# Optimization experiments

Measured on AMD Instinct MI355X. Metric: run time of the kernel, lower is better.

## Reference

```python
import jax, jax.numpy as jnp
import numpy as np

N, D_MODEL, D_PE, H = 4096, 512, 16, 8


def setup_inputs() -> dict:
    key = jax.random.key(0)
    ks = jax.random.split(key, 6)
    s = 1.0 / np.sqrt(D_MODEL)
    return {
        "x": jax.random.normal(ks[0], (N, D_MODEL), dtype=jnp.float32),
        "pe": jax.random.normal(ks[1], (N, D_PE), dtype=jnp.float32),
        "w_qkv": jax.random.normal(ks[2], (D_MODEL, 3 * D_MODEL), dtype=jnp.float32) * s,
        "b_qkv": jnp.zeros((3 * D_MODEL,), dtype=jnp.float32),
        "w_pe": jax.random.normal(ks[3], (D_PE, H), dtype=jnp.float32) * (1.0 / np.sqrt(D_PE)),
        "b_pe": jnp.zeros((H,), dtype=jnp.float32),
        "w_out": jax.random.normal(ks[4], (D_MODEL, D_MODEL), dtype=jnp.float32) * s,
        "b_out": jnp.zeros((D_MODEL,), dtype=jnp.float32),
    }


def reference(x, pe, w_qkv, b_qkv, w_pe, b_pe, w_out, b_out):
    n, d = x.shape
    h = w_pe.shape[1]
    hd = d // h
    scale = hd ** -0.5

    qkv = (x @ w_qkv + b_qkv).reshape(n, 3, h, hd)  # [N,3,H,hd]
    q = jnp.transpose(qkv[:, 0], (1, 0, 2))  # [H,N,hd]
    k = jnp.transpose(qkv[:, 1], (1, 0, 2))
    v = jnp.transpose(qkv[:, 2], (1, 0, 2))

    pe_proj = pe @ w_pe + b_pe  # [N,H]
    # bias[h,i,j] = pe_proj[j,h] - pe_proj[i,h]  (matches torch unsqueeze/permute)
    pt = pe_proj.T  # [H,N]
    bias = pt[:, None, :] - pt[:, :, None]  # [H,N,N]

    scores = jnp.einsum('hnd,hmd->hnm', q, k) * scale + bias  # [H,N,N]
    attn = jax.nn.softmax(scores, axis=-1)
    out = jnp.einsum('hnm,hmd->hnd', attn, v)  # [H,N,hd]
    out = jnp.transpose(out, (1, 0, 2)).reshape(n, d)
    return out @ w_out + b_out
```

## Files before the change

kernel.cpp:

```cpp
#include <hip/hip_runtime.h>
#include <stdint.h>
#include <stddef.h>


typedef unsigned short u16;
typedef __attribute__((ext_vector_type(8))) short short8;
typedef __attribute__((ext_vector_type(8))) unsigned short us8;
typedef __attribute__((ext_vector_type(4))) unsigned short us4;
typedef __attribute__((ext_vector_type(4))) float floatx4;

__device__ __forceinline__ u16 f2b(float f) {
  union { float f; uint32_t u; } v; v.f = f;
  uint32_t u = v.u;
  return (u16)((u + 0x7fffu + ((u >> 16) & 1u)) >> 16);
}

__device__ __forceinline__ uint32_t pkbf16(float a, float b) {
  union { float f; uint32_t u; } x, y; x.f = a; y.f = b;
  return __builtin_amdgcn_perm(y.u + 0x8000u, x.u + 0x8000u, 0x07060302u);
}

#if __has_builtin(__builtin_amdgcn_exp2f)
__device__ __forceinline__ float fexp2(float x) { return __builtin_amdgcn_exp2f(x); }
#else
__device__ __forceinline__ float fexp2(float x) { return exp2f(x); }
#endif

__device__ __forceinline__ void gld16(const u16* g, u16* l) {
  __builtin_amdgcn_global_load_lds(
      (const __attribute__((address_space(1))) uint32_t*)(const void*)g,
      (__attribute__((address_space(3))) uint32_t*)(void*)l, 16, 0, 0);
}


__device__ __forceinline__ void tr_tile(const float* __restrict__ in,
                                        u16* __restrict__ out, int R, int C,
                                        int bx, int by, u16 (*tile)[33]) {
  int tx = threadIdx.x & 31, ty = threadIdx.x >> 5;
  int c0 = bx * 32, r0 = by * 32;
#pragma unroll
  for (int i = 0; i < 32; i += 8)
    tile[ty + i][tx] = f2b(in[(size_t)(r0 + ty + i) * C + c0 + tx]);
  __syncthreads();
#pragma unroll
  for (int i = 0; i < 32; i += 8)
    out[(size_t)(c0 + ty + i) * R + r0 + tx] = tile[tx][ty + i];
}

__global__ __launch_bounds__(256) void k_prep(
    const float* __restrict__ x, u16* __restrict__ xb,
    const float* __restrict__ w_qkv, u16* __restrict__ wqkvT,
    const float* __restrict__ w_out, u16* __restrict__ woutT,
    const float* __restrict__ pe, const float* __restrict__ w_pe,
    const float* __restrict__ b_pe, float* __restrict__ peT) {
  __shared__ u16 tile[32][33];
  int b = blockIdx.x;
  if (b < 2048) {
    int i = b * 256 + threadIdx.x;
    float4 v = ((const float4*)x)[i];
    uint2 o = make_uint2(pkbf16(v.x, v.y), pkbf16(v.z, v.w));
    ((uint2*)xb)[i] = o;
  } else if (b < 2816) {
    int idx = b - 2048;
    tr_tile(w_qkv, wqkvT, 512, 1536, idx % 48, idx / 48, tile);
  } else if (b < 3072) {
    int idx = b - 2816;
    tr_tile(w_out, woutT, 512, 512, idx % 16, idx / 16, tile);
  } else {
    int idx = (b - 3072) * 256 + threadIdx.x;
    int h = idx >> 12, n = idx & 4095;
    float acc = b_pe[h];
#pragma unroll
    for (int d = 0; d < 16; ++d) acc = fmaf(pe[n * 16 + d], w_pe[d * 8 + h], acc);
    peT[h * 4096 + n] = acc * 1.4426950408889634f - 16.0f;
  }
}


__global__ __launch_bounds__(512, 6) void k_gemm_qkv(const u16* __restrict__ A,
                                                     const u16* __restrict__ Bt,
                                                     const float* __restrict__ bias,
                                                     u16* __restrict__ qk,
                                                     u16* __restrict__ vtp) {
  __shared__ __align__(16) u16 smem[24576];
  const int tid = threadIdx.x;
  const int lane = tid & 63, wave = tid >> 6;
  const int colx = lane & 15, quad = lane >> 4;
  const int m0 = blockIdx.y * 64, n0 = blockIdx.x * 128;
  const int wm = wave >> 2, wn = wave & 3;
  const int sc = (lane & 7) ^ ((lane >> 3) & 7);
  const floatx4 fz = {0.f, 0.f, 0.f, 0.f};
  floatx4 acc[2][2];
#pragma unroll
  for (int i = 0; i < 2; ++i)
#pragma unroll
    for (int j = 0; j < 2; ++j) acc[i][j] = fz;

#define PREF_QKV(k0, b)                                                       \
  {                                                                           \
    int rowa = wave * 8 + (lane >> 3);                                        \
    gld16(&A[(size_t)(m0 + rowa) * 512 + (k0) + sc * 8],                      \
          &smem[(b) * 4096 + wave * 512 + lane * 8]);                         \
    _Pragma("unroll") for (int c = 0; c < 2; ++c) {                           \
      int rowb = wave * 16 + c * 8 + (lane >> 3);                             \
      gld16(&Bt[(size_t)(n0 + rowb) * 512 + (k0) + sc * 8],                   \
            &smem[8192 + (b) * 8192 + wave * 1024 + c * 512 + lane * 8]);     \
    }                                                                         \
  }

  PREF_QKV(0, 0);
  __syncthreads();
  for (int it = 0; it < 8; ++it) {
    int cur = it & 1;
    if (it < 7) PREF_QKV((it + 1) * 64, cur ^ 1);
    const u16* As = &smem[cur * 4096];
    const u16* Bs = &smem[8192 + cur * 8192];
#pragma unroll
    for (int kk = 0; kk < 2; ++kk) {
      short8 af[2], bf[2];
#pragma unroll
      for (int i = 0; i < 2; ++i) {
        int row = wm * 32 + i * 16 + colx;
        af[i] = *(const short8*)&As[row * 64 + (((kk * 4 + quad) ^ (colx & 7))) * 8];
      }
#pragma unroll
      for (int j = 0; j < 2; ++j) {
        int row = wn * 32 + j * 16 + colx;
        bf[j] = *(const short8*)&Bs[row * 64 + (((kk * 4 + quad) ^ (colx & 7))) * 8];
      }
#pragma unroll
      for (int i = 0; i < 2; ++i)
#pragma unroll
        for (int j = 0; j < 2; ++j)
          acc[i][j] = __builtin_amdgcn_mfma_f32_16x16x32_bf16(af[i], bf[j], acc[i][j], 0, 0, 0);
    }
    __syncthreads();
  }

  const bool isV = (blockIdx.x >= 8);
#pragma unroll
  for (int j = 0; j < 2; ++j) {
    int c = n0 + wn * 32 + j * 16 + colx;
    float bq = bias[c];
    if (!isV) {
#pragma unroll
      for (int i = 0; i < 2; ++i)
#pragma unroll
        for (int r = 0; r < 4; ++r) {
          int row = m0 + wm * 32 + i * 16 + quad * 4 + r;
          qk[(size_t)row * 1024 + c] = f2b(acc[i][j][r] + bq);
        }
    } else {
      int d = c - 1024;
#pragma unroll
      for (int i = 0; i < 2; ++i) {
        us4 o;
#pragma unroll
        for (int r = 0; r < 4; ++r) o[r] = f2b(acc[i][j][r] + bq);
        *(us4*)&vtp[(size_t)d * 4096 + m0 + wm * 32 + quad * 8 + i * 4] = o;
      }
    }
  }
#undef PREF_QKV
}


__global__ __launch_bounds__(512, 4) void k_gemm_out(const u16* __restrict__ A,
                                                     const u16* __restrict__ Bt,
                                                     const float* __restrict__ bias,
                                                     float* __restrict__ Cout) {
  __shared__ __align__(16) u16 smem[16384];
  const int tid = threadIdx.x;
  const int lane = tid & 63, wave = tid >> 6;
  const int colx = lane & 15, quad = lane >> 4;
  const int m0 = blockIdx.y * 64, n0 = blockIdx.x * 64;
  const int wm = wave >> 2, wn = wave & 3;
  const int sc = (lane & 7) ^ ((lane >> 3) & 7);
  const floatx4 fz = {0.f, 0.f, 0.f, 0.f};
  floatx4 acc[2];
  acc[0] = fz; acc[1] = fz;

#define PREF_OUT(k0, b)                                                       \
  {                                                                           \
    int rowa = wave * 8 + (lane >> 3);                                        \
    gld16(&A[(size_t)(m0 + rowa) * 512 + (k0) + sc * 8],                      \
          &smem[(b) * 4096 + wave * 512 + lane * 8]);                         \
    gld16(&Bt[(size_t)(n0 + rowa) * 512 + (k0) + sc * 8],                     \
          &smem[8192 + (b) * 4096 + wave * 512 + lane * 8]);                  \
  }

  PREF_OUT(0, 0);
  __syncthreads();
  for (int it = 0; it < 8; ++it) {
    int cur = it & 1;
    if (it < 7) PREF_OUT((it + 1) * 64, cur ^ 1);
    const u16* As = &smem[cur * 4096];
    const u16* Bs = &smem[8192 + cur * 4096];
#pragma unroll
    for (int kk = 0; kk < 2; ++kk) {
      short8 af[2], bf;
#pragma unroll
      for (int i = 0; i < 2; ++i) {
        int row = wm * 32 + i * 16 + colx;
        af[i] = *(const short8*)&As[row * 64 + (((kk * 4 + quad) ^ (colx & 7))) * 8];
      }
      {
        int row = wn * 16 + colx;
        bf = *(const short8*)&Bs[row * 64 + (((kk * 4 + quad) ^ (colx & 7))) * 8];
      }
#pragma unroll
      for (int i = 0; i < 2; ++i)
        acc[i] = __builtin_amdgcn_mfma_f32_16x16x32_bf16(af[i], bf, acc[i], 0, 0, 0);
    }
    __syncthreads();
  }
  int c = n0 + wn * 16 + colx;
  float bq = bias[c];
#pragma unroll
  for (int i = 0; i < 2; ++i)
#pragma unroll
    for (int r = 0; r < 4; ++r) {
      int row = m0 + wm * 32 + i * 16 + quad * 4 + r;
      Cout[(size_t)row * 512 + c] = acc[i][r] + bq;
    }
#undef PREF_OUT
}


__global__ __launch_bounds__(512, 8) void k_flash(const u16* __restrict__ qk,
                                                  const u16* __restrict__ vt,
                                                  const float* __restrict__ peT,
                                                  float* __restrict__ opart,
                                                  float* __restrict__ lpart) {
  __shared__ __align__(16) u16 smem[20480];
  float* bufs = (float*)smem;

  const int tid = threadIdx.x;
  const int lane = tid & 63, wave = tid >> 6;
  const int colx = lane & 15, quad = lane >> 4;
  const int ih = wave >> 1, jq = wave & 1;
  const int q0 = blockIdx.x * 64;
  const int h = blockIdx.y;
  const int z = blockIdx.z;
  const int kvb = z * 2048;
  const float sscale = 0.125f * 1.4426950408889634f;
  const floatx4 fz = {0.f, 0.f, 0.f, 0.f};

  const int sc = (lane & 7) ^ ((lane >> 3) & 7);
  const int srow = wave * 8 + (lane >> 3);

#define PREF_F(j0n, b)                                                        \
  {                                                                           \
    gld16(&qk[(size_t)(kvb + (j0n) + srow) * 1024 + 512 + h * 64 + sc * 8],   \
          &smem[4096 + (b) * 4096 + wave * 512 + lane * 8]);                  \
    gld16(&vt[(size_t)(h * 64 + srow) * 4096 + kvb + (j0n) + sc * 8],         \
          &smem[12288 + (b) * 4096 + wave * 512 + lane * 8]);                 \
  }

  {
    int row = tid >> 3, ch = tid & 7;
    *(us8*)&smem[row * 64 + (ch ^ (row & 7)) * 8] =
        *(const us8*)&qk[(size_t)(q0 + row) * 1024 + h * 64 + ch * 8];
  }
  PREF_F(0, 0);
  __syncthreads();

  short8 qf[2];
#pragma unroll
  for (int kk = 0; kk < 2; ++kk) {
    int row = ih * 16 + colx;
    qf[kk] = *(const short8*)&smem[row * 64 + (((kk * 4 + quad) ^ (colx & 7))) * 8];
  }

  floatx4 oacc[4];
#pragma unroll
  for (int cb = 0; cb < 4; ++cb) oacc[cb] = fz;
  float rsum = 0.0f;

  for (int it = 0; it < 32; ++it) {
    const int cur = it & 1;
    if (it < 31) PREF_F((it + 1) * 64, cur ^ 1);
    const u16* Ks = &smem[4096 + cur * 4096];
    const u16* Vts = &smem[12288 + cur * 4096];

    floatx4 pev[2];
#pragma unroll
    for (int j2 = 0; j2 < 2; ++j2)
      pev[j2] = *(const floatx4*)&peT[h * 4096 + kvb + it * 64 + jq * 32 + j2 * 16 + quad * 4];

    floatx4 sacc[2] = {fz, fz};
#pragma unroll
    for (int j2 = 0; j2 < 2; ++j2) {
#pragma unroll
      for (int kk = 0; kk < 2; ++kk) {
        int row = jq * 32 + j2 * 16 + colx;
        short8 kf = *(const short8*)&Ks[row * 64 + (((kk * 4 + quad) ^ (colx & 7))) * 8];
        sacc[j2] = __builtin_amdgcn_mfma_f32_16x16x32_bf16(kf, qf[kk], sacc[j2], 0, 0, 0);
      }
    }
    union { uint32_t w[4]; short8 s; } pk;
#pragma unroll
    for (int j2 = 0; j2 < 2; ++j2) {
      float p0 = fexp2(fmaf(sacc[j2][0], sscale, pev[j2][0]));
      float p1 = fexp2(fmaf(sacc[j2][1], sscale, pev[j2][1]));
      float p2 = fexp2(fmaf(sacc[j2][2], sscale, pev[j2][2]));
      float p3 = fexp2(fmaf(sacc[j2][3], sscale, pev[j2][3]));
      rsum += (p0 + p1) + (p2 + p3);
      pk.w[j2 * 2 + 0] = pkbf16(p0, p1);
      pk.w[j2 * 2 + 1] = pkbf16(p2, p3);
    }
#pragma unroll
    for (int cb = 0; cb < 4; ++cb) {
      int row = cb * 16 + colx;
      short8 vf = *(const short8*)&Vts[row * 64 + (((jq * 4 + quad) ^ (colx & 7))) * 8];
      oacc[cb] = __builtin_amdgcn_mfma_f32_16x16x32_bf16(pk.s, vf, oacc[cb], 0, 0, 0);
    }
    __syncthreads();
  }

  rsum += __shfl_xor(rsum, 16);
  rsum += __shfl_xor(rsum, 32);

  float* b = bufs + ih * 1040;
  if (jq == 1) {
#pragma unroll
    for (int cb = 0; cb < 4; ++cb)
#pragma unroll
      for (int r = 0; r < 4; ++r)
        b[(quad * 4 + r) * 65 + cb * 16 + colx] = oacc[cb][r];
    if (quad == 0) b[colx * 65 + 64] = rsum;
  }
  __syncthreads();
  if (jq == 0) {
#pragma unroll
    for (int cb = 0; cb < 4; ++cb)
#pragma unroll
      for (int r = 0; r < 4; ++r)
        oacc[cb][r] += b[(quad * 4 + r) * 65 + cb * 16 + colx];
    rsum += b[colx * 65 + 64];
    float* op = opart + (size_t)z * 2097152;
#pragma unroll
    for (int cb = 0; cb < 4; ++cb)
#pragma unroll
      for (int r = 0; r < 4; ++r)
        op[(size_t)(q0 + ih * 16 + quad * 4 + r) * 512 + h * 64 + cb * 16 + colx] =
            oacc[cb][r];
    if (quad == 0)
      lpart[z * 32768 + h * 4096 + q0 + ih * 16 + colx] = rsum;
  }
#undef PREF_F
}


__global__ __launch_bounds__(256) void k_comb(const float* __restrict__ opart,
                                              const float* __restrict__ lpart,
                                              u16* __restrict__ ao) {
  int idx = blockIdx.x * 256 + threadIdx.x;
  int n = idx >> 7, d4 = idx & 127;
  int h = d4 >> 4;
  float l = lpart[h * 4096 + n] + lpart[32768 + h * 4096 + n];
  float inv = 1.0f / l;
  float4 o0 = *(const float4*)&opart[(size_t)n * 512 + d4 * 4];
  float4 o1 = *(const float4*)&opart[2097152 + (size_t)n * 512 + d4 * 4];
  us4 o;
  o[0] = f2b((o0.x + o1.x) * inv);
  o[1] = f2b((o0.y + o1.y) * inv);
  o[2] = f2b((o0.z + o1.z) * inv);
  o[3] = f2b((o0.w + o1.w) * inv);
  *(us4*)&ao[(size_t)n * 512 + d4 * 4] = o;
}


extern "C" void kernel_launch(void* const* d_in, const int* in_sizes, int n_in,
                              void* d_out, int out_size, void* d_ws, size_t ws_size,
                              hipStream_t stream) {
  const float* x     = (const float*)d_in[0];
  const float* pe    = (const float*)d_in[1];
  const float* w_qkv = (const float*)d_in[2];
  const float* b_qkv = (const float*)d_in[3];
  const float* w_pe  = (const float*)d_in[4];
  const float* b_pe  = (const float*)d_in[5];
  const float* w_out = (const float*)d_in[6];
  const float* b_out = (const float*)d_in[7];
  float* out = (float*)d_out;

  u16* xb    = (u16*)d_ws;
  u16* wqkvT = xb    + 2097152;
  u16* woutT = wqkvT + 786432;
  u16* qk    = woutT + 262144;
  u16* vt    = qk    + 4194304;
  u16* ao    = vt    + 2097152;
  float* peT   = (float*)(ao + 2097152);
  float* opart = peT + 32768;
  float* lpart = opart + 4194304;

  k_prep<<<3200, 256, 0, stream>>>(x, xb, w_qkv, wqkvT, w_out, woutT,
                                   pe, w_pe, b_pe, peT);
  k_gemm_qkv<<<dim3(12, 64), 512, 0, stream>>>(xb, wqkvT, b_qkv, qk, vt);
  k_flash<<<dim3(64, 8, 2), 512, 0, stream>>>(qk, vt, peT, opart, lpart);
  k_comb<<<2048, 256, 0, stream>>>(opart, lpart, ao);
  k_gemm_out<<<dim3(8, 64), 512, 0, stream>>>(ao, woutT, b_out, out);
}
```

Baseline: 152.5 us.

## Fold positional bias into V weights, MFMA row sums, fuse combine into out GEMM

Because bias[i,j] = p[j] - p[i], the per-query term cancels in softmax and the per-key term becomes a multiplicative weight exp(p[j]). The change folds that weight into V in the QKV GEMM epilogue and folds the score scale into Q. The flash loop therefore drops its per-tile peT loads and FMAs, and the softmax denominator is computed with an extra MFMA against a bf16 weight vector instead of scalar adds. The separate combine kernel is removed by normalising and merging the split-K partials while loading A tiles in the output GEMM. The cost is extra bf16 rounding of the weights and of the scaled V and Q, and A tiles in the out GEMM are now loaded synchronously through registers.

Result: slower. 159.8 us (+4.8%).

```diff
diff --git a/kernel.cpp b/kernel.cpp
--- a/kernel.cpp
+++ b/kernel.cpp
@@ -52,7 +52,8 @@
     const float* __restrict__ w_qkv, u16* __restrict__ wqkvT,
     const float* __restrict__ w_out, u16* __restrict__ woutT,
     const float* __restrict__ pe, const float* __restrict__ w_pe,
-    const float* __restrict__ b_pe, float* __restrict__ peT) {
+    const float* __restrict__ b_pe, float* __restrict__ wexp,
+    u16* __restrict__ wpb) {
   __shared__ u16 tile[32][33];
   int b = blockIdx.x;
   if (b < 2048) {
@@ -72,7 +73,12 @@
     float acc = b_pe[h];
 #pragma unroll
     for (int d = 0; d < 16; ++d) acc = fmaf(pe[n * 16 + d], w_pe[d * 8 + h], acc);
-    peT[h * 4096 + n] = acc * 1.4426950408889634f - 16.0f;
+    float w = exp2f(acc * 1.4426950408889634f - 16.0f);
+    u16 wb = f2b(w);
+    union { uint32_t u; float f; } cv; cv.u = ((uint32_t)wb) << 16;
+    wexp[h * 4096 + n] = cv.f;
+    int pn = (n & ~31) | (((n >> 2) & 3) << 3) | (((n >> 4) & 1) << 2) | (n & 3);
+    wpb[h * 4096 + pn] = wb;
   }
 }
 
@@ -80,6 +86,7 @@
 __global__ __launch_bounds__(512, 6) void k_gemm_qkv(const u16* __restrict__ A,
                                                      const u16* __restrict__ Bt,
                                                      const float* __restrict__ bias,
+                                                     const float* __restrict__ wexp,
                                                      u16* __restrict__ qk,
                                                      u16* __restrict__ vtp) {
   __shared__ __align__(16) u16 smem[24576];
@@ -143,20 +150,25 @@
     int c = n0 + wn * 32 + j * 16 + colx;
     float bq = bias[c];
     if (!isV) {
+      float qs = (c < 512) ? 0.18033688011112042f : 1.0f;
 #pragma unroll
       for (int i = 0; i < 2; ++i)
 #pragma unroll
         for (int r = 0; r < 4; ++r) {
           int row = m0 + wm * 32 + i * 16 + quad * 4 + r;
-          qk[(size_t)row * 1024 + c] = f2b(acc[i][j][r] + bq);
+          qk[(size_t)row * 1024 + c] = f2b((acc[i][j][r] + bq) * qs);
         }
     } else {
       int d = c - 1024;
+      int hh = (n0 + wn * 32 + j * 16 - 1024) >> 6;
 #pragma unroll
       for (int i = 0; i < 2; ++i) {
         us4 o;
 #pragma unroll
-        for (int r = 0; r < 4; ++r) o[r] = f2b(acc[i][j][r] + bq);
+        for (int r = 0; r < 4; ++r) {
+          int na = m0 + wm * 32 + i * 16 + quad * 4 + r;
+          o[r] = f2b((acc[i][j][r] + bq) * wexp[hh * 4096 + na]);
+        }
         *(us4*)&vtp[(size_t)d * 4096 + m0 + wm * 32 + quad * 8 + i * 4] = o;
       }
     }
@@ -165,7 +177,136 @@
 }
 
 
-__global__ __launch_bounds__(512, 4) void k_gemm_out(const u16* __restrict__ A,
+__global__ __launch_bounds__(512, 8) void k_flash(const u16* __restrict__ qk,
+                                                  const u16* __restrict__ vt,
+                                                  const u16* __restrict__ wpb,
+                                                  float* __restrict__ opart,
+                                                  float* __restrict__ lpart) {
+  __shared__ __align__(16) u16 smem[20480];
+  float* bufs = (float*)smem;
+
+  const int tid = threadIdx.x;
+  const int lane = tid & 63, wave = tid >> 6;
+  const int colx = lane & 15, quad = lane >> 4;
+  const int ih = wave >> 1, jq = wave & 1;
+  const int q0 = blockIdx.x * 64;
+  const int h = blockIdx.y;
+  const int z = blockIdx.z;
+  const int kvb = z * 2048;
+  const floatx4 fz = {0.f, 0.f, 0.f, 0.f};
+
+  const int sc = (lane & 7) ^ ((lane >> 3) & 7);
+  const int srow = wave * 8 + (lane >> 3);
+
+#define PREF_F(j0n, b)                                                        \
+  {                                                                           \
+    gld16(&qk[(size_t)(kvb + (j0n) + srow) * 1024 + 512 + h * 64 + sc * 8],   \
+          &smem[4096 + (b) * 4096 + wave * 512 + lane * 8]);                  \
+    gld16(&vt[(size_t)(h * 64 + srow) * 4096 + kvb + (j0n) + sc * 8],         \
+          &smem[12288 + (b) * 4096 + wave * 512 + lane * 8]);                 \
+  }
+
+  {
+    int row = tid >> 3, ch = tid & 7;
+    *(us8*)&smem[row * 64 + (ch ^ (row & 7)) * 8] =
+        *(const us8*)&qk[(size_t)(q0 + row) * 1024 + h * 64 + ch * 8];
+  }
+  PREF_F(0, 0);
+  __syncthreads();
+
+  short8 qf[2];
+#pragma unroll
+  for (int kk = 0; kk < 2; ++kk) {
+    int row = ih * 16 + colx;
+    qf[kk] = *(const short8*)&smem[row * 64 + (((kk * 4 + quad) ^ (colx & 7))) * 8];
+  }
+
+  const u16* wbase = wpb + h * 4096 + kvb + jq * 32 + quad * 8;
+  short8 wf = *(const short8*)wbase;
+
+  floatx4 oacc[4], lacc = fz;
+#pragma unroll
+  for (int cb = 0; cb < 4; ++cb) oacc[cb] = fz;
+
+  for (int it = 0; it < 32; ++it) {
+    const int cur = it & 1;
+    short8 wfn;
+    if (it < 31) {
+      PREF_F((it + 1) * 64, cur ^ 1);
+      wfn = *(const short8*)&wbase[(it + 1) * 64];
+    }
+    const u16* Ks = &smem[4096 + cur * 4096];
+    const u16* Vts = &smem[12288 + cur * 4096];
+
+    floatx4 sacc[2] = {fz, fz};
+#pragma unroll
+    for (int j2 = 0; j2 < 2; ++j2) {
+#pragma unroll
+      for (int kk = 0; kk < 2; ++kk) {
+        int row = jq * 32 + j2 * 16 + colx;
+        short8 kf = *(const short8*)&Ks[row * 64 + (((kk * 4 + quad) ^ (colx & 7))) * 8];
+        sacc[j2] = __builtin_amdgcn_mfma_f32_16x16x32_bf16(kf, qf[kk], sacc[j2], 0, 0, 0);
+      }
+    }
+    union { uint32_t w[4]; short8 s; } pk;
+#pragma unroll
+    for (int j2 = 0; j2 < 2; ++j2) {
+      float p0 = fexp2(sacc[j2][0]);
+      float p1 = fexp2(sacc[j2][1]);
+      float p2 = fexp2(sacc[j2][2]);
+      float p3 = fexp2(sacc[j2][3]);
+      pk.w[j2 * 2 + 0] = pkbf16(p0, p1);
+      pk.w[j2 * 2 + 1] = pkbf16(p2, p3);
+    }
+#pragma unroll
+    for (int cb = 0; cb < 4; ++cb) {
+      int row = cb * 16 + colx;
+      short8 vf = *(const short8*)&Vts[row * 64 + (((jq * 4 + quad) ^ (colx & 7))) * 8];
+      oacc[cb] = __builtin_amdgcn_mfma_f32_16x16x32_bf16(pk.s, vf, oacc[cb], 0, 0, 0);
+    }
+    lacc = __builtin_amdgcn_mfma_f32_16x16x32_bf16(pk.s, wf, lacc, 0, 0, 0);
+    if (it < 31) wf = wfn;
+    __syncthreads();
+  }
+
+  float* b = bufs + ih * 1040;
+  if (jq == 1) {
+#pragma unroll
+    for (int cb = 0; cb < 4; ++cb)
+#pragma unroll
+      for (int r = 0; r < 4; ++r)
+        b[(quad * 4 + r) * 65 + cb * 16 + colx] = oacc[cb][r];
+    if (colx == 0)
+#pragma unroll
+      for (int r = 0; r < 4; ++r) b[(quad * 4 + r) * 65 + 64] = lacc[r];
+  }
+  __syncthreads();
+  if (jq == 0) {
+#pragma unroll
+    for (int cb = 0; cb < 4; ++cb)
+#pragma unroll
+      for (int r = 0; r < 4; ++r)
+        oacc[cb][r] += b[(quad * 4 + r) * 65 + cb * 16 + colx];
+#pragma unroll
+    for (int r = 0; r < 4; ++r) lacc[r] += b[(quad * 4 + r) * 65 + 64];
+    float* op = opart + (size_t)z * 2097152;
+#pragma unroll
+    for (int cb = 0; cb < 4; ++cb)
+#pragma unroll
+      for (int r = 0; r < 4; ++r)
+        op[(size_t)(q0 + ih * 16 + quad * 4 + r) * 512 + h * 64 + cb * 16 + colx] =
+            oacc[cb][r];
+    if (colx == 0)
+#pragma unroll
+      for (int r = 0; r < 4; ++r)
+        lpart[z * 32768 + h * 4096 + q0 + ih * 16 + quad * 4 + r] = lacc[r];
+  }
+#undef PREF_F
+}
+
+
+__global__ __launch_bounds__(512, 4) void k_gemm_out(const float* __restrict__ opart,
+                                                     const float* __restrict__ lpart,
                                                      const u16* __restrict__ Bt,
                                                      const float* __restrict__ bias,
                                                      float* __restrict__ Cout) {
@@ -176,24 +317,42 @@
   const int m0 = blockIdx.y * 64, n0 = blockIdx.x * 64;
   const int wm = wave >> 2, wn = wave & 3;
   const int sc = (lane & 7) ^ ((lane >> 3) & 7);
+  const int rowa = wave * 8 + (lane >> 3);
+  const int na = m0 + rowa;
   const floatx4 fz = {0.f, 0.f, 0.f, 0.f};
   floatx4 acc[2];
   acc[0] = fz; acc[1] = fz;
 
-#define PREF_OUT(k0, b)                                                       \
+#define LOADA(k0)                                                             \
   {                                                                           \
-    int rowa = wave * 8 + (lane >> 3);                                        \
-    gld16(&A[(size_t)(m0 + rowa) * 512 + (k0) + sc * 8],                      \
-          &smem[(b) * 4096 + wave * 512 + lane * 8]);                         \
-    gld16(&Bt[(size_t)(n0 + rowa) * 512 + (k0) + sc * 8],                     \
-          &smem[8192 + (b) * 4096 + wave * 512 + lane * 8]);                  \
-  }
-
-  PREF_OUT(0, 0);
+    int dbase = (k0) + sc * 8;                                                \
+    const float4* p0 = (const float4*)&opart[(size_t)na * 512 + dbase];       \
+    const float4* p1 = (const float4*)&opart[2097152 + (size_t)na * 512 + dbase]; \
+    a0 = p0[0]; a1 = p0[1]; c0 = p1[0]; c1 = p1[1];                           \
+    int hh = dbase >> 6;                                                      \
+    li = 1.0f / (lpart[hh * 4096 + na] + lpart[32768 + hh * 4096 + na]);      \
+  }
+#define PACKA(b)                                                              \
+  {                                                                           \
+    union { uint32_t w[4]; us8 v; } pa;                                       \
+    pa.w[0] = pkbf16((a0.x + c0.x) * li, (a0.y + c0.y) * li);                 \
+    pa.w[1] = pkbf16((a0.z + c0.z) * li, (a0.w + c0.w) * li);                 \
+    pa.w[2] = pkbf16((a1.x + c1.x) * li, (a1.y + c1.y) * li);                 \
+    pa.w[3] = pkbf16((a1.z + c1.z) * li, (a1.w + c1.w) * li);                 \
+    *(us8*)&smem[(b) * 4096 + wave * 512 + lane * 8] = pa.v;                  \
+  }
+
+  float4 a0, a1, c0, c1; float li;
+  LOADA(0); PACKA(0);
+  gld16(&Bt[(size_t)(n0 + rowa) * 512 + sc * 8], &smem[8192 + wave * 512 + lane * 8]);
   __syncthreads();
   for (int it = 0; it < 8; ++it) {
     int cur = it & 1;
-    if (it < 7) PREF_OUT((it + 1) * 64, cur ^ 1);
+    if (it < 7) {
+      LOADA((it + 1) * 64);
+      gld16(&Bt[(size_t)(n0 + rowa) * 512 + (it + 1) * 64 + sc * 8],
+            &smem[8192 + (cur ^ 1) * 4096 + wave * 512 + lane * 8]);
+    }
     const u16* As = &smem[cur * 4096];
     const u16* Bs = &smem[8192 + cur * 4096];
 #pragma unroll
@@ -212,6 +371,7 @@
       for (int i = 0; i < 2; ++i)
         acc[i] = __builtin_amdgcn_mfma_f32_16x16x32_bf16(af[i], bf, acc[i], 0, 0, 0);
     }
+    if (it < 7) PACKA(cur ^ 1);
     __syncthreads();
   }
   int c = n0 + wn * 16 + colx;
@@ -223,151 +383,8 @@
       int row = m0 + wm * 32 + i * 16 + quad * 4 + r;
       Cout[(size_t)row * 512 + c] = acc[i][r] + bq;
     }
-#undef PREF_OUT
-}
-
-
-__global__ __launch_bounds__(512, 8) void k_flash(const u16* __restrict__ qk,
-                                                  const u16* __restrict__ vt,
-                                                  const float* __restrict__ peT,
-                                                  float* __restrict__ opart,
-                                                  float* __restrict__ lpart) {
-  __shared__ __align__(16) u16 smem[20480];
-  float* bufs = (float*)smem;
-
-  const int tid = threadIdx.x;
-  const int lane = tid & 63, wave = tid >> 6;
-  const int colx = lane & 15, quad = lane >> 4;
-  const int ih = wave >> 1, jq = wave & 1;
-  const int q0 = blockIdx.x * 64;
-  const int h = blockIdx.y;
-  const int z = blockIdx.z;
-  const int kvb = z * 2048;
-  const float sscale = 0.125f * 1.4426950408889634f;
-  const floatx4 fz = {0.f, 0.f, 0.f, 0.f};
-
-  const int sc = (lane & 7) ^ ((lane >> 3) & 7);
-  const int srow = wave * 8 + (lane >> 3);
-
-#define PREF_F(j0n, b)                                                        \
-  {                                                                           \
-    gld16(&qk[(size_t)(kvb + (j0n) + srow) * 1024 + 512 + h * 64 + sc * 8],   \
-          &smem[4096 + (b) * 4096 + wave * 512 + lane * 8]);                  \
-    gld16(&vt[(size_t)(h * 64 + srow) * 4096 + kvb + (j0n) + sc * 8],         \
-          &smem[12288 + (b) * 4096 + wave * 512 + lane * 8]);                 \
-  }
-
-  {
-    int row = tid >> 3, ch = tid & 7;
-    *(us8*)&smem[row * 64 + (ch ^ (row & 7)) * 8] =
-        *(const us8*)&qk[(size_t)(q0 + row) * 1024 + h * 64 + ch * 8];
-  }
-  PREF_F(0, 0);
-  __syncthreads();
-
-  short8 qf[2];
-#pragma unroll
-  for (int kk = 0; kk < 2; ++kk) {
-    int row = ih * 16 + colx;
-    qf[kk] = *(const short8*)&smem[row * 64 + (((kk * 4 + quad) ^ (colx & 7))) * 8];
-  }
-
-  floatx4 oacc[4];
-#pragma unroll
-  for (int cb = 0; cb < 4; ++cb) oacc[cb] = fz;
-  float rsum = 0.0f;
-
-  for (int it = 0; it < 32; ++it) {
-    const int cur = it & 1;
-    if (it < 31) PREF_F((it + 1) * 64, cur ^ 1);
-    const u16* Ks = &smem[4096 + cur * 4096];
-    const u16* Vts = &smem[12288 + cur * 4096];
-
-    floatx4 pev[2];
-#pragma unroll
-    for (int j2 = 0; j2 < 2; ++j2)
-      pev[j2] = *(const floatx4*)&peT[h * 4096 + kvb + it * 64 + jq * 32 + j2 * 16 + quad * 4];
-
-    floatx4 sacc[2] = {fz, fz};
-#pragma unroll
-    for (int j2 = 0; j2 < 2; ++j2) {
-#pragma unroll
-      for (int kk = 0; kk < 2; ++kk) {
-        int row = jq * 32 + j2 * 16 + colx;
-        short8 kf = *(const short8*)&Ks[row * 64 + (((kk * 4 + quad) ^ (colx & 7))) * 8];
-        sacc[j2] = __builtin_amdgcn_mfma_f32_16x16x32_bf16(kf, qf[kk], sacc[j2], 0, 0, 0);
-      }
-    }
-    union { uint32_t w[4]; short8 s; } pk;
-#pragma unroll
-    for (int j2 = 0; j2 < 2; ++j2) {
-      float p0 = fexp2(fmaf(sacc[j2][0], sscale, pev[j2][0]));
-      float p1 = fexp2(fmaf(sacc[j2][1], sscale, pev[j2][1]));
-      float p2 = fexp2(fmaf(sacc[j2][2], sscale, pev[j2][2]));
-      float p3 = fexp2(fmaf(sacc[j2][3], sscale, pev[j2][3]));
-      rsum += (p0 + p1) + (p2 + p3);
-      pk.w[j2 * 2 + 0] = pkbf16(p0, p1);
-      pk.w[j2 * 2 + 1] = pkbf16(p2, p3);
-    }
-#pragma unroll
-    for (int cb = 0; cb < 4; ++cb) {
-      int row = cb * 16 + colx;
-      short8 vf = *(const short8*)&Vts[row * 64 + (((jq * 4 + quad) ^ (colx & 7))) * 8];
-      oacc[cb] = __builtin_amdgcn_mfma_f32_16x16x32_bf16(pk.s, vf, oacc[cb], 0, 0, 0);
-    }
-    __syncthreads();
-  }
-
-  rsum += __shfl_xor(rsum, 16);
-  rsum += __shfl_xor(rsum, 32);
-
-  float* b = bufs + ih * 1040;
-  if (jq == 1) {
-#pragma unroll
-    for (int cb = 0; cb < 4; ++cb)
-#pragma unroll
-      for (int r = 0; r < 4; ++r)
-        b[(quad * 4 + r) * 65 + cb * 16 + colx] = oacc[cb][r];
-    if (quad == 0) b[colx * 65 + 64] = rsum;
-  }
-  __syncthreads();
-  if (jq == 0) {
-#pragma unroll
-    for (int cb = 0; cb < 4; ++cb)
-#pragma unroll
-      for (int r = 0; r < 4; ++r)
-        oacc[cb][r] += b[(quad * 4 + r) * 65 + cb * 16 + colx];
-    rsum += b[colx * 65 + 64];
-    float* op = opart + (size_t)z * 2097152;
-#pragma unroll
-    for (int cb = 0; cb < 4; ++cb)
-#pragma unroll
-      for (int r = 0; r < 4; ++r)
-        op[(size_t)(q0 + ih * 16 + quad * 4 + r) * 512 + h * 64 + cb * 16 + colx] =
-            oacc[cb][r];
-    if (quad == 0)
-      lpart[z * 32768 + h * 4096 + q0 + ih * 16 + colx] = rsum;
-  }
-#undef PREF_F
-}
-
-
-__global__ __launch_bounds__(256) void k_comb(const float* __restrict__ opart,
-                                              const float* __restrict__ lpart,
-                                              u16* __restrict__ ao) {
-  int idx = blockIdx.x * 256 + threadIdx.x;
-  int n = idx >> 7, d4 = idx & 127;
-  int h = d4 >> 4;
-  float l = lpart[h * 4096 + n] + lpart[32768 + h * 4096 + n];
-  float inv = 1.0f / l;
-  float4 o0 = *(const float4*)&opart[(size_t)n * 512 + d4 * 4];
-  float4 o1 = *(const float4*)&opart[2097152 + (size_t)n * 512 + d4 * 4];
-  us4 o;
-  o[0] = f2b((o0.x + o1.x) * inv);
-  o[1] = f2b((o0.y + o1.y) * inv);
-  o[2] = f2b((o0.z + o1.z) * inv);
-  o[3] = f2b((o0.w + o1.w) * inv);
-  *(us4*)&ao[(size_t)n * 512 + d4 * 4] = o;
+#undef LOADA
+#undef PACKA
 }
 
 
@@ -389,15 +406,14 @@
   u16* woutT = wqkvT + 786432;
   u16* qk    = woutT + 262144;
   u16* vt    = qk    + 4194304;
-  u16* ao    = vt    + 2097152;
-  float* peT   = (float*)(ao + 2097152);
-  float* opart = peT + 32768;
+  u16* wpb   = vt    + 2097152;
+  float* wexp  = (float*)(wpb + 32768);
+  float* opart = wexp + 32768;
   float* lpart = opart + 4194304;
 
   k_prep<<<3200, 256, 0, stream>>>(x, xb, w_qkv, wqkvT, w_out, woutT,
-                                   pe, w_pe, b_pe, peT);
-  k_gemm_qkv<<<dim3(12, 64), 512, 0, stream>>>(xb, wqkvT, b_qkv, qk, vt);
-  k_flash<<<dim3(64, 8, 2), 512, 0, stream>>>(qk, vt, peT, opart, lpart);
-  k_comb<<<2048, 256, 0, stream>>>(opart, lpart, ao);
-  k_gemm_out<<<dim3(8, 64), 512, 0, stream>>>(ao, woutT, b_out, out);
-}
+                                   pe, w_pe, b_pe, wexp, wpb);
+  k_gemm_qkv<<<dim3(12, 64), 512, 0, stream>>>(xb, wqkvT, b_qkv, wexp, qk, vt);
+  k_flash<<<dim3(64, 8, 2), 512, 0, stream>>>(qk, vt, wpb, opart, lpart);
+  k_gemm_out<<<dim3(8, 64), 512, 0, stream>>>(opart, lpart, woutT, b_out, out);
+}
```

## Fold positional bias into V scaling and compute row sums via MFMA

Applied to the files above, without the earlier changes.

The positional bias pe_proj[j]-pe_proj[i] is factored out of the softmax. The key-side term becomes an exp weight folded into V during the QKV GEMM epilogue. The query-side term cancels under normalization. The softmax scale is folded into Q, so the flash inner loop drops the per-element FMA and bias loads. Row sums are computed by an extra MFMA against a permuted bf16 weight vector instead of scalar adds, and the main loop is unrolled by two with pointer increments. The cost is extra bf16 rounding of the weights and scaled V, plus one more MFMA per tile.

New measurement: 146.4 us. -4.0%, faster.

```diff
diff --git a/kernel.cpp b/kernel.cpp
--- a/kernel.cpp
+++ b/kernel.cpp
@@ -52,7 +52,8 @@
     const float* __restrict__ w_qkv, u16* __restrict__ wqkvT,
     const float* __restrict__ w_out, u16* __restrict__ woutT,
     const float* __restrict__ pe, const float* __restrict__ w_pe,
-    const float* __restrict__ b_pe, float* __restrict__ peT) {
+    const float* __restrict__ b_pe, float* __restrict__ wexp,
+    u16* __restrict__ wpb) {
   __shared__ u16 tile[32][33];
   int b = blockIdx.x;
   if (b < 2048) {
@@ -72,7 +73,12 @@
     float acc = b_pe[h];
 #pragma unroll
     for (int d = 0; d < 16; ++d) acc = fmaf(pe[n * 16 + d], w_pe[d * 8 + h], acc);
-    peT[h * 4096 + n] = acc * 1.4426950408889634f - 16.0f;
+    float w = exp2f(acc * 1.4426950408889634f - 16.0f);
+    u16 wb = f2b(w);
+    union { uint32_t u; float f; } cv; cv.u = ((uint32_t)wb) << 16;
+    wexp[h * 4096 + n] = cv.f;
+    int pn = (n & ~31) | (((n >> 2) & 3) << 3) | (((n >> 4) & 1) << 2) | (n & 3);
+    wpb[h * 4096 + pn] = wb;
   }
 }
 
@@ -80,6 +86,7 @@
 __global__ __launch_bounds__(512, 6) void k_gemm_qkv(const u16* __restrict__ A,
                                                      const u16* __restrict__ Bt,
                                                      const float* __restrict__ bias,
+                                                     const float* __restrict__ wexp,
                                                      u16* __restrict__ qk,
                                                      u16* __restrict__ vtp) {
   __shared__ __align__(16) u16 smem[24576];
@@ -138,17 +145,25 @@
   }
 
   const bool isV = (blockIdx.x >= 8);
+  floatx4 wv[2];
+  if (isV) {
+    int hh = (n0 + wn * 32 - 1024) >> 6;
+#pragma unroll
+    for (int i = 0; i < 2; ++i)
+      wv[i] = *(const floatx4*)&wexp[hh * 4096 + m0 + wm * 32 + i * 16 + quad * 4];
+  }
 #pragma unroll
   for (int j = 0; j < 2; ++j) {
     int c = n0 + wn * 32 + j * 16 + colx;
     float bq = bias[c];
     if (!isV) {
+      float qs = (c < 512) ? 0.18033688011112042f : 1.0f;
 #pragma unroll
       for (int i = 0; i < 2; ++i)
 #pragma unroll
         for (int r = 0; r < 4; ++r) {
           int row = m0 + wm * 32 + i * 16 + quad * 4 + r;
-          qk[(size_t)row * 1024 + c] = f2b(acc[i][j][r] + bq);
+          qk[(size_t)row * 1024 + c] = f2b((acc[i][j][r] + bq) * qs);
         }
     } else {
       int d = c - 1024;
@@ -156,7 +171,8 @@
       for (int i = 0; i < 2; ++i) {
         us4 o;
 #pragma unroll
-        for (int r = 0; r < 4; ++r) o[r] = f2b(acc[i][j][r] + bq);
+        for (int r = 0; r < 4; ++r)
+          o[r] = f2b((acc[i][j][r] + bq) * wv[i][r]);
         *(us4*)&vtp[(size_t)d * 4096 + m0 + wm * 32 + quad * 8 + i * 4] = o;
       }
     }
@@ -165,71 +181,9 @@
 }
 
 
-__global__ __launch_bounds__(512, 4) void k_gemm_out(const u16* __restrict__ A,
-                                                     const u16* __restrict__ Bt,
-                                                     const float* __restrict__ bias,
-                                                     float* __restrict__ Cout) {
-  __shared__ __align__(16) u16 smem[16384];
-  const int tid = threadIdx.x;
-  const int lane = tid & 63, wave = tid >> 6;
-  const int colx = lane & 15, quad = lane >> 4;
-  const int m0 = blockIdx.y * 64, n0 = blockIdx.x * 64;
-  const int wm = wave >> 2, wn = wave & 3;
-  const int sc = (lane & 7) ^ ((lane >> 3) & 7);
-  const floatx4 fz = {0.f, 0.f, 0.f, 0.f};
-  floatx4 acc[2];
-  acc[0] = fz; acc[1] = fz;
-
-#define PREF_OUT(k0, b)                                                       \
-  {                                                                           \
-    int rowa = wave * 8 + (lane >> 3);                                        \
-    gld16(&A[(size_t)(m0 + rowa) * 512 + (k0) + sc * 8],                      \
-          &smem[(b) * 4096 + wave * 512 + lane * 8]);                         \
-    gld16(&Bt[(size_t)(n0 + rowa) * 512 + (k0) + sc * 8],                     \
-          &smem[8192 + (b) * 4096 + wave * 512 + lane * 8]);                  \
-  }
-
-  PREF_OUT(0, 0);
-  __syncthreads();
-  for (int it = 0; it < 8; ++it) {
-    int cur = it & 1;
-    if (it < 7) PREF_OUT((it + 1) * 64, cur ^ 1);
-    const u16* As = &smem[cur * 4096];
-    const u16* Bs = &smem[8192 + cur * 4096];
-#pragma unroll
-    for (int kk = 0; kk < 2; ++kk) {
-      short8 af[2], bf;
-#pragma unroll
-      for (int i = 0; i < 2; ++i) {
-        int row = wm * 32 + i * 16 + colx;
-        af[i] = *(const short8*)&As[row * 64 + (((kk * 4 + quad) ^ (colx & 7))) * 8];
-      }
-      {
-        int row = wn * 16 + colx;
-        bf = *(const short8*)&Bs[row * 64 + (((kk * 4 + quad) ^ (colx & 7))) * 8];
-      }
-#pragma unroll
-      for (int i = 0; i < 2; ++i)
-        acc[i] = __builtin_amdgcn_mfma_f32_16x16x32_bf16(af[i], bf, acc[i], 0, 0, 0);
-    }
-    __syncthreads();
-  }
-  int c = n0 + wn * 16 + colx;
-  float bq = bias[c];
-#pragma unroll
-  for (int i = 0; i < 2; ++i)
-#pragma unroll
-    for (int r = 0; r < 4; ++r) {
-      int row = m0 + wm * 32 + i * 16 + quad * 4 + r;
-      Cout[(size_t)row * 512 + c] = acc[i][r] + bq;
-    }
-#undef PREF_OUT
-}
-
-
 __global__ __launch_bounds__(512, 8) void k_flash(const u16* __restrict__ qk,
                                                   const u16* __restrict__ vt,
-                                                  const float* __restrict__ peT,
+                                                  const u16* __restrict__ wpb,
                                                   float* __restrict__ opart,
                                                   float* __restrict__ lpart) {
   __shared__ __align__(16) u16 smem[20480];
@@ -243,26 +197,23 @@
   const int h = blockIdx.y;
   const int z = blockIdx.z;
   const int kvb = z * 2048;
-  const float sscale = 0.125f * 1.4426950408889634f;
   const floatx4 fz = {0.f, 0.f, 0.f, 0.f};
 
   const int sc = (lane & 7) ^ ((lane >> 3) & 7);
   const int srow = wave * 8 + (lane >> 3);
-
-#define PREF_F(j0n, b)                                                        \
-  {                                                                           \
-    gld16(&qk[(size_t)(kvb + (j0n) + srow) * 1024 + 512 + h * 64 + sc * 8],   \
-          &smem[4096 + (b) * 4096 + wave * 512 + lane * 8]);                  \
-    gld16(&vt[(size_t)(h * 64 + srow) * 4096 + kvb + (j0n) + sc * 8],         \
-          &smem[12288 + (b) * 4096 + wave * 512 + lane * 8]);                 \
-  }
 
   {
     int row = tid >> 3, ch = tid & 7;
     *(us8*)&smem[row * 64 + (ch ^ (row & 7)) * 8] =
         *(const us8*)&qk[(size_t)(q0 + row) * 1024 + h * 64 + ch * 8];
   }
-  PREF_F(0, 0);
+  const u16* qptr = qk + (size_t)(kvb + srow) * 1024 + 512 + h * 64 + sc * 8;
+  const u16* vptr = vt + (size_t)(h * 64 + srow) * 4096 + kvb + sc * 8;
+  const u16* wptr = wpb + h * 4096 + kvb + jq * 32 + quad * 8;
+  gld16(qptr, &smem[4096 + wave * 512 + lane * 8]);
+  gld16(vptr, &smem[12288 + wave * 512 + lane * 8]);
+  qptr += 65536;
+  vptr += 64;
   __syncthreads();
 
   short8 qf[2];
@@ -272,54 +223,59 @@
     qf[kk] = *(const short8*)&smem[row * 64 + (((kk * 4 + quad) ^ (colx & 7))) * 8];
   }
 
-  floatx4 oacc[4];
+  floatx4 oacc[4], lacc = fz;
 #pragma unroll
   for (int cb = 0; cb < 4; ++cb) oacc[cb] = fz;
-  float rsum = 0.0f;
-
-  for (int it = 0; it < 32; ++it) {
-    const int cur = it & 1;
-    if (it < 31) PREF_F((it + 1) * 64, cur ^ 1);
-    const u16* Ks = &smem[4096 + cur * 4096];
-    const u16* Vts = &smem[12288 + cur * 4096];
-
-    floatx4 pev[2];
-#pragma unroll
-    for (int j2 = 0; j2 < 2; ++j2)
-      pev[j2] = *(const floatx4*)&peT[h * 4096 + kvb + it * 64 + jq * 32 + j2 * 16 + quad * 4];
-
-    floatx4 sacc[2] = {fz, fz};
-#pragma unroll
-    for (int j2 = 0; j2 < 2; ++j2) {
-#pragma unroll
-      for (int kk = 0; kk < 2; ++kk) {
-        int row = jq * 32 + j2 * 16 + colx;
-        short8 kf = *(const short8*)&Ks[row * 64 + (((kk * 4 + quad) ^ (colx & 7))) * 8];
-        sacc[j2] = __builtin_amdgcn_mfma_f32_16x16x32_bf16(kf, qf[kk], sacc[j2], 0, 0, 0);
-      }
-    }
-    union { uint32_t w[4]; short8 s; } pk;
-#pragma unroll
-    for (int j2 = 0; j2 < 2; ++j2) {
-      float p0 = fexp2(fmaf(sacc[j2][0], sscale, pev[j2][0]));
-      float p1 = fexp2(fmaf(sacc[j2][1], sscale, pev[j2][1]));
-      float p2 = fexp2(fmaf(sacc[j2][2], sscale, pev[j2][2]));
-      float p3 = fexp2(fmaf(sacc[j2][3], sscale, pev[j2][3]));
-      rsum += (p0 + p1) + (p2 + p3);
-      pk.w[j2 * 2 + 0] = pkbf16(p0, p1);
-      pk.w[j2 * 2 + 1] = pkbf16(p2, p3);
-    }
-#pragma unroll
-    for (int cb = 0; cb < 4; ++cb) {
-      int row = cb * 16 + colx;
-      short8 vf = *(const short8*)&Vts[row * 64 + (((jq * 4 + quad) ^ (colx & 7))) * 8];
-      oacc[cb] = __builtin_amdgcn_mfma_f32_16x16x32_bf16(pk.s, vf, oacc[cb], 0, 0, 0);
-    }
-    __syncthreads();
-  }
-
-  rsum += __shfl_xor(rsum, 16);
-  rsum += __shfl_xor(rsum, 32);
+
+#define FBODY(CUR, PREF)                                                      \
+  {                                                                           \
+    short8 wf = *(const short8*)wptr;                                         \
+    wptr += 64;                                                               \
+    if (PREF) {                                                               \
+      gld16(qptr, &smem[4096 + (1 - (CUR)) * 4096 + wave * 512 + lane * 8]);  \
+      gld16(vptr, &smem[12288 + (1 - (CUR)) * 4096 + wave * 512 + lane * 8]); \
+      qptr += 65536;                                                          \
+      vptr += 64;                                                             \
+    }                                                                         \
+    const u16* Ks = &smem[4096 + (CUR) * 4096];                               \
+    const u16* Vts = &smem[12288 + (CUR) * 4096];                             \
+    floatx4 sacc[2] = {fz, fz};                                               \
+    _Pragma("unroll") for (int j2 = 0; j2 < 2; ++j2) {                        \
+      _Pragma("unroll") for (int kk = 0; kk < 2; ++kk) {                      \
+        int row = jq * 32 + j2 * 16 + colx;                                   \
+        short8 kf = *(const short8*)&Ks[row * 64 +                            \
+                                        (((kk * 4 + quad) ^ (colx & 7))) * 8];\
+        sacc[j2] =                                                            \
+            __builtin_amdgcn_mfma_f32_16x16x32_bf16(kf, qf[kk], sacc[j2], 0, 0, 0); \
+      }                                                                       \
+    }                                                                         \
+    union { uint32_t w[4]; short8 s; } pk;                                    \
+    _Pragma("unroll") for (int j2 = 0; j2 < 2; ++j2) {                        \
+      float p0 = fexp2(sacc[j2][0]);                                          \
+      float p1 = fexp2(sacc[j2][1]);                                          \
+      float p2 = fexp2(sacc[j2][2]);                                          \
+      float p3 = fexp2(sacc[j2][3]);                                          \
+      pk.w[j2 * 2 + 0] = pkbf16(p0, p1);                                      \
+      pk.w[j2 * 2 + 1] = pkbf16(p2, p3);                                      \
+    }                                                                         \
+    _Pragma("unroll") for (int cb = 0; cb < 4; ++cb) {                        \
+      int row = cb * 16 + colx;                                               \
+      short8 vf = *(const short8*)&Vts[row * 64 +                             \
+                                       (((jq * 4 + quad) ^ (colx & 7))) * 8]; \
+      oacc[cb] =                                                              \
+          __builtin_amdgcn_mfma_f32_16x16x32_bf16(pk.s, vf, oacc[cb], 0, 0, 0); \
+    }                                                                         \
+    lacc = __builtin_amdgcn_mfma_f32_16x16x32_bf16(pk.s, wf, lacc, 0, 0, 0);  \
+    __syncthreads();                                                          \
+  }
+
+  for (int t = 0; t < 15; ++t) {
+    FBODY(0, 1)
+    FBODY(1, 1)
+  }
+  FBODY(0, 1)
+  FBODY(1, 0)
+#undef FBODY
 
   float* b = bufs + ih * 1040;
   if (jq == 1) {
@@ -328,7 +284,9 @@
 #pragma unroll
       for (int r = 0; r < 4; ++r)
         b[(quad * 4 + r) * 65 + cb * 16 + colx] = oacc[cb][r];
-    if (quad == 0) b[colx * 65 + 64] = rsum;
+    if (colx == 0)
+#pragma unroll
+      for (int r = 0; r < 4; ++r) b[(quad * 4 + r) * 65 + 64] = lacc[r];
   }
   __syncthreads();
   if (jq == 0) {
@@ -337,7 +295,8 @@
 #pragma unroll
       for (int r = 0; r < 4; ++r)
         oacc[cb][r] += b[(quad * 4 + r) * 65 + cb * 16 + colx];
-    rsum += b[colx * 65 + 64];
+#pragma unroll
+    for (int r = 0; r < 4; ++r) lacc[r] += b[(quad * 4 + r) * 65 + 64];
     float* op = opart + (size_t)z * 2097152;
 #pragma unroll
     for (int cb = 0; cb < 4; ++cb)
@@ -345,10 +304,11 @@
       for (int r = 0; r < 4; ++r)
         op[(size_t)(q0 + ih * 16 + quad * 4 + r) * 512 + h * 64 + cb * 16 + colx] =
             oacc[cb][r];
-    if (quad == 0)
-      lpart[z * 32768 + h * 4096 + q0 + ih * 16 + colx] = rsum;
-  }
-#undef PREF_F
+    if (colx == 0)
+#pragma unroll
+      for (int r = 0; r < 4; ++r)
+        lpart[z * 32768 + h * 4096 + q0 + ih * 16 + quad * 4 + r] = lacc[r];
+  }
 }
 
 
@@ -371,6 +331,68 @@
 }
 
 
+__global__ __launch_bounds__(512, 4) void k_gemm_out(const u16* __restrict__ A,
+                                                     const u16* __restrict__ Bt,
+                                                     const float* __restrict__ bias,
+                                                     float* __restrict__ Cout) {
+  __shared__ __align__(16) u16 smem[16384];
+  const int tid = threadIdx.x;
+  const int lane = tid & 63, wave = tid >> 6;
+  const int colx = lane & 15, quad = lane >> 4;
+  const int m0 = blockIdx.y * 64, n0 = blockIdx.x * 64;
+  const int wm = wave >> 2, wn = wave & 3;
+  const int sc = (lane & 7) ^ ((lane >> 3) & 7);
+  const floatx4 fz = {0.f, 0.f, 0.f, 0.f};
+  floatx4 acc[2];
+  acc[0] = fz; acc[1] = fz;
+
+#define PREF_OUT(k0, b)                                                       \
+  {                                                                           \
+    int rowa = wave * 8 + (lane >> 3);                                        \
+    gld16(&A[(size_t)(m0 + rowa) * 512 + (k0) + sc * 8],                      \
+          &smem[(b) * 4096 + wave * 512 + lane * 8]);                         \
+    gld16(&Bt[(size_t)(n0 + rowa) * 512 + (k0) + sc * 8],                     \
+          &smem[8192 + (b) * 4096 + wave * 512 + lane * 8]);                  \
+  }
+
+  PREF_OUT(0, 0);
+  __syncthreads();
+  for (int it = 0; it < 8; ++it) {
+    int cur = it & 1;
+    if (it < 7) PREF_OUT((it + 1) * 64, cur ^ 1);
+    const u16* As = &smem[cur * 4096];
+    const u16* Bs = &smem[8192 + cur * 4096];
+#pragma unroll
+    for (int kk = 0; kk < 2; ++kk) {
+      short8 af[2], bf;
+#pragma unroll
+      for (int i = 0; i < 2; ++i) {
+        int row = wm * 32 + i * 16 + colx;
+        af[i] = *(const short8*)&As[row * 64 + (((kk * 4 + quad) ^ (colx & 7))) * 8];
+      }
+      {
+        int row = wn * 16 + colx;
+        bf = *(const short8*)&Bs[row * 64 + (((kk * 4 + quad) ^ (colx & 7))) * 8];
+      }
+#pragma unroll
+      for (int i = 0; i < 2; ++i)
+        acc[i] = __builtin_amdgcn_mfma_f32_16x16x32_bf16(af[i], bf, acc[i], 0, 0, 0);
+    }
+    __syncthreads();
+  }
+  int c = n0 + wn * 16 + colx;
+  float bq = bias[c];
+#pragma unroll
+  for (int i = 0; i < 2; ++i)
+#pragma unroll
+    for (int r = 0; r < 4; ++r) {
+      int row = m0 + wm * 32 + i * 16 + quad * 4 + r;
+      Cout[(size_t)row * 512 + c] = acc[i][r] + bq;
+    }
+#undef PREF_OUT
+}
+
+
 extern "C" void kernel_launch(void* const* d_in, const int* in_sizes, int n_in,
                               void* d_out, int out_size, void* d_ws, size_t ws_size,
                               hipStream_t stream) {
@@ -389,15 +411,16 @@
   u16* woutT = wqkvT + 786432;
   u16* qk    = woutT + 262144;
   u16* vt    = qk    + 4194304;
-  u16* ao    = vt    + 2097152;
-  float* peT   = (float*)(ao + 2097152);
-  float* opart = peT + 32768;
+  u16* wpb   = vt    + 2097152;
+  u16* ao    = wpb   + 32768;
+  float* wexp  = (float*)(ao + 2097152);
+  float* opart = wexp + 32768;
   float* lpart = opart + 4194304;
 
   k_prep<<<3200, 256, 0, stream>>>(x, xb, w_qkv, wqkvT, w_out, woutT,
-                                   pe, w_pe, b_pe, peT);
-  k_gemm_qkv<<<dim3(12, 64), 512, 0, stream>>>(xb, wqkvT, b_qkv, qk, vt);
-  k_flash<<<dim3(64, 8, 2), 512, 0, stream>>>(qk, vt, peT, opart, lpart);
+                                   pe, w_pe, b_pe, wexp, wpb);
+  k_gemm_qkv<<<dim3(12, 64), 512, 0, stream>>>(xb, wqkvT, b_qkv, wexp, qk, vt);
+  k_flash<<<dim3(64, 8, 2), 512, 0, stream>>>(qk, vt, wpb, opart, lpart);
   k_comb<<<2048, 256, 0, stream>>>(opart, lpart, ao);
   k_gemm_out<<<dim3(8, 64), 512, 0, stream>>>(ao, woutT, b_out, out);
 }
```
